# Performance work log

Hardware: AMD Instinct MI355X
Metric: run time of the kernel (lower is better)

Reference implementation:

```python
import jax, jax.numpy as jnp
import numpy as np

DECAY = 0.8
EPS = 1e-05


def setup_inputs() -> dict:
    key = jax.random.key(0)
    k_x, k_e = jax.random.split(key)
    x = jax.random.normal(k_x, (8, 4096, 256), dtype=jnp.float32)
    embed = jax.random.normal(k_e, (8192, 256), dtype=jnp.float32)
    cluster_size = jnp.zeros((8192,), dtype=jnp.float32)
    embed_avg = embed  # buffer initialized as embed.clone()
    return {"x": x, "embed": embed, "cluster_size": cluster_size, "embed_avg": embed_avg}


def reference(x, embed, cluster_size, embed_avg):
    shape = x.shape
    K, d = embed.shape
    flatten = x.reshape(-1, d)  # [N, d]

    dist = -(jnp.sum(flatten * flatten, axis=1, keepdims=True)
             - 2.0 * (flatten @ embed.T)
             + jnp.sum(embed * embed, axis=1)[None, :])  # [N, K]
    embed_ind = jnp.argmax(dist, axis=-1)  # [N]

    quantize = jnp.take(embed, embed_ind, axis=0).reshape(shape)
    embed_ind_out = embed_ind.reshape(shape[:-1])

    # Training-mode EMA update (one_hot sum / one_hot matmul expressed as scatter-adds)
    counts = jnp.zeros((K,), dtype=x.dtype).at[embed_ind].add(1.0)  # embed_onehot.sum(0)
    embed_sum = jnp.zeros((K, d), dtype=x.dtype).at[embed_ind].add(flatten)  # (flatten^T @ onehot)^T

    new_cluster_size = cluster_size * DECAY + counts * (1.0 - DECAY)
    new_embed_avg = embed_avg * DECAY + embed_sum * (1.0 - DECAY)

    smoothed = (new_cluster_size + EPS) / (new_cluster_size.sum() + K * EPS) * new_cluster_size.sum()
    new_embed = new_embed_avg / smoothed[:, None]

    return quantize, embed_ind_out, new_cluster_size, new_embed_avg, new_embed
```

## Files before the change

kernel.cpp:

```cpp
#include <hip/hip_runtime.h>

#define N_ROWS 32768
#define DIM    256
#define KCODES 8192
#define DECAYF 0.8f
#define OMDF   0.2f
#define EPSF   1e-5f

#define Q_OFF    0
#define IND_OFF  8388608
#define CS_OFF   8421376
#define EA_OFF   8429568
#define NE_OFF   10526720


#define WS_E2    0
#define WS_CNT   8192
#define WS_START 16384
#define WS_CUR   24576
#define WS_SUM   40960

typedef _Float16 half8 __attribute__((ext_vector_type(8)));
typedef float floatx16 __attribute__((ext_vector_type(16)));

#define GLOAD16(g, l) __builtin_amdgcn_global_load_lds( \
    (const __attribute__((address_space(1))) void*)(g), \
    (__attribute__((address_space(3))) void*)(l), 16, 0, 0)

#define PREP_ROWS 32
__global__ void prep_all_kernel(const float* __restrict__ x,
                                const float* __restrict__ embed,
                                const float* __restrict__ cs,
                                _Float16* __restrict__ Xp,
                                _Float16* __restrict__ Ep,
                                float* __restrict__ out,
                                float* __restrict__ ws) {
  __shared__ __align__(16) _Float16 L[PREP_ROWS][264];
  __shared__ float red[4];
  const int t = threadIdx.x;
  const int bid = blockIdx.x;

  if (bid < 1024) {
    if (bid < 128) {
      unsigned long long* gbest = (unsigned long long*)(out + EA_OFF);
      gbest[bid * 256 + t] = 0ULL;
    } else if (bid < 160) {
      ((int*)(ws + WS_CNT))[(bid - 128) * 256 + t] = 0;
    }
    const int row0 = bid * PREP_ROWS;
    #pragma unroll
    for (int it = 0; it < 8; ++it) {
      int idx = it * 256 + t;
      int r = idx >> 6, q = idx & 63;
      float4 v = *(const float4*)&x[(size_t)(row0 + r) * DIM + q * 4];
      L[r][q * 4 + 0] = (_Float16)v.x;
      L[r][q * 4 + 1] = (_Float16)v.y;
      L[r][q * 4 + 2] = (_Float16)v.z;
      L[r][q * 4 + 3] = (_Float16)v.w;
    }
    __syncthreads();
    #pragma unroll
    for (int it = 0; it < 4; ++it) {
      int idx = it * 256 + t;
      int slot = idx >> 5, r = idx & 31;
      *(float4*)&Xp[((size_t)slot * N_ROWS + row0 + r) * 8] =
          *(const float4*)&L[r][slot * 8];
    }
  } else {
    const int row0 = (bid - 1024) * PREP_ROWS;
    float* e2 = ws + WS_E2;
    #pragma unroll
    for (int it = 0; it < 8; ++it) {
      int idx = it * 256 + t;
      int r = idx >> 6, q = idx & 63;
      float4 v = *(const float4*)&embed[(size_t)(row0 + r) * DIM + q * 4];
      L[r][q * 4 + 0] = (_Float16)v.x;
      L[r][q * 4 + 1] = (_Float16)v.y;
      L[r][q * 4 + 2] = (_Float16)v.z;
      L[r][q * 4 + 3] = (_Float16)v.w;
      float ssq = v.x * v.x + v.y * v.y + v.z * v.z + v.w * v.w;
      #pragma unroll
      for (int o = 32; o; o >>= 1) ssq += __shfl_xor(ssq, o);
      if ((t & 63) == 0) e2[row0 + r] = ssq;
    }
    if (bid == 1024) {
      float s = 0.0f;
      for (int j = t; j < KCODES; j += 256) s += cs[j];
      #pragma unroll
      for (int o = 32; o; o >>= 1) s += __shfl_xor(s, o);
      if ((t & 63) == 0) red[t >> 6] = s;
    }
    __syncthreads();
    if (bid == 1024 && t == 0)
      ws[WS_SUM] = red[0] + red[1] + red[2] + red[3];
    #pragma unroll
    for (int it = 0; it < 4; ++it) {
      int idx = it * 256 + t;
      int slot = idx >> 5, r = idx & 31;
      *(float4*)&Ep[((size_t)slot * KCODES + row0 + r) * 8] =
          *(const float4*)&L[r][slot * 8];
    }
  }
}

__global__ __launch_bounds__(512, 2) void main_kernel(
    const _Float16* __restrict__ Xp, const _Float16* __restrict__ Ep,
    const float* __restrict__ e2, unsigned long long* __restrict__ gbest) {
  __shared__ __align__(16) _Float16 As[4 * 2 * 256 * 8];
  __shared__ __align__(16) _Float16 Bs[4 * 2 * 256 * 8];
  __shared__ __align__(16) float e2s[256];

  const int t = threadIdx.x;
  const int w = t >> 6;
  const int lane = t & 63;
  const int l31 = lane & 31;
  const int h = lane >> 5;
  const int wm = w >> 2;
  const int wn = w & 3;

  const int bid = blockIdx.x;
  const int bi = bid >> 3;
  const int cb = (bid & 7) * 4 + (bi >> 5);
  const int rbg = bi & 31;
  const int codes0 = cb * 256;
  const int rowbase = rbg * 1024;

  const bool isA = (w < 4);
  const int ws4 = isA ? w : (w - 4);
  const int sl = ws4 >> 1;
  const int qh = ws4 & 1;

  auto stage = [&](int s) {
    const int buf = s & 3;
    const int se = (s & 15) * 2 + sl;
    if (isA) {
      const _Float16* src =
          Ep + ((size_t)se * KCODES + codes0 + qh * 128 + lane) * 8;
      _Float16* dst = &As[buf * 4096 + sl * 2048 + qh * 1024];
      GLOAD16(src, dst);
      GLOAD16(src + 512, dst + 512);
    } else {
      const int row0 = rowbase + (s >> 4) * 256;
      const _Float16* src =
          Xp + ((size_t)se * N_ROWS + row0 + qh * 128 + lane) * 8;
      _Float16* dst = &Bs[buf * 4096 + sl * 2048 + qh * 1024];
      GLOAD16(src, dst);
      GLOAD16(src + 512, dst + 512);
    }
  };

  if (t < 64) {
    float4 v = *(const float4*)&e2[codes0 + t * 4];
    *(float4*)&e2s[t * 4] = v;
  }
  __builtin_amdgcn_sched_barrier(0);
  stage(0);
  stage(1);
  asm volatile("s_waitcnt vmcnt(2)" ::: "memory");
  asm volatile("s_waitcnt lgkmcnt(0)" ::: "memory");
  __builtin_amdgcn_s_barrier();
  __builtin_amdgcn_sched_barrier(0);

  floatx16 acc[4][2];
  unsigned long long pbest[4][2];

  #pragma unroll
  for (int tile = 0; tile < 4; ++tile) {
    #pragma unroll
    for (int ct = 0; ct < 4; ++ct) {
      const int cl = wm * 128 + ct * 32 + 4 * h;
      #pragma unroll
      for (int rq = 0; rq < 4; ++rq) {
        float4 v = *(const float4*)&e2s[cl + rq * 8];
        acc[ct][0][rq * 4 + 0] = -0.5f * v.x;
        acc[ct][0][rq * 4 + 1] = -0.5f * v.y;
        acc[ct][0][rq * 4 + 2] = -0.5f * v.z;
        acc[ct][0][rq * 4 + 3] = -0.5f * v.w;
      }
      acc[ct][1] = acc[ct][0];
    }

    #pragma unroll 1
    for (int i = 0; i < 16; ++i) {
      const int s = tile * 16 + i;
      if (s + 2 < 64) stage(s + 2);
      __builtin_amdgcn_sched_barrier(0);

      const int sbase = (s & 3) * 4096 + h * 2048;
      half8 a0 = *(const half8*)&As[sbase + (wm * 128 + l31) * 8];
      half8 a1 = *(const half8*)&As[sbase + (wm * 128 + 32 + l31) * 8];
      half8 a2 = *(const half8*)&As[sbase + (wm * 128 + 64 + l31) * 8];
      half8 a3 = *(const half8*)&As[sbase + (wm * 128 + 96 + l31) * 8];
      half8 b0 = *(const half8*)&Bs[sbase + (wn * 64 + l31) * 8];
      half8 b1 = *(const half8*)&Bs[sbase + (wn * 64 + 32 + l31) * 8];
      __builtin_amdgcn_s_setprio(1);
      acc[0][0] = __builtin_amdgcn_mfma_f32_32x32x16_f16(a0, b0, acc[0][0], 0, 0, 0);
      acc[0][1] = __builtin_amdgcn_mfma_f32_32x32x16_f16(a0, b1, acc[0][1], 0, 0, 0);
      acc[1][0] = __builtin_amdgcn_mfma_f32_32x32x16_f16(a1, b0, acc[1][0], 0, 0, 0);
      acc[1][1] = __builtin_amdgcn_mfma_f32_32x32x16_f16(a1, b1, acc[1][1], 0, 0, 0);
      acc[2][0] = __builtin_amdgcn_mfma_f32_32x32x16_f16(a2, b0, acc[2][0], 0, 0, 0);
      acc[2][1] = __builtin_amdgcn_mfma_f32_32x32x16_f16(a2, b1, acc[2][1], 0, 0, 0);
      acc[3][0] = __builtin_amdgcn_mfma_f32_32x32x16_f16(a3, b0, acc[3][0], 0, 0, 0);
      acc[3][1] = __builtin_amdgcn_mfma_f32_32x32x16_f16(a3, b1, acc[3][1], 0, 0, 0);
      __builtin_amdgcn_s_setprio(0);
      __builtin_amdgcn_sched_barrier(0);

      if (s < 63) {
        if (s < 62) {
          asm volatile("s_waitcnt vmcnt(2)" ::: "memory");
        } else {
          asm volatile("s_waitcnt vmcnt(0)" ::: "memory");
        }
        __builtin_amdgcn_s_barrier();
        __builtin_amdgcn_sched_barrier(0);
      }
    }

    #pragma unroll
    for (int rt = 0; rt < 2; ++rt) {
      float best = -3.0e38f;
      int bidx = 0;
      #pragma unroll
      for (int ct = 0; ct < 4; ++ct) {
        const int cbase = codes0 + wm * 128 + ct * 32 + 4 * h;
        #pragma unroll
        for (int r = 0; r < 16; ++r) {
          const int code = cbase + (r & 3) + 8 * (r >> 2);
          float v = acc[ct][rt][r];
          if (v > best || (v == best && code < bidx)) { best = v; bidx = code; }
        }
      }
      unsigned u = __float_as_uint(best);
      u = (u & 0x80000000u) ? ~u : (u | 0x80000000u);
      unsigned long long p =
          ((unsigned long long)u << 32) | (unsigned)(8191 - bidx);
      unsigned long long op = (unsigned long long)__shfl_xor((long long)p, 32);
      if (op > p) p = op;
      pbest[tile][rt] = p;
    }
  }

  #pragma unroll
  for (int tile = 0; tile < 4; ++tile)
    #pragma unroll
    for (int rt = 0; rt < 2; ++rt)
      if (h == 0)
        atomicMax(&gbest[rowbase + tile * 256 + wn * 64 + rt * 32 + l31],
                  pbest[tile][rt]);
}

__global__ void decode_count_kernel(const unsigned long long* __restrict__ gbest,
                                    float* __restrict__ out,
                                    int* __restrict__ cnt) {
  int r = blockIdx.x * blockDim.x + threadIdx.x;
  unsigned long long p = gbest[r];
  int k = 8191 - (int)(unsigned)(p & 0xFFFFFFFFull);
  out[IND_OFF + r] = (float)k;
  atomicAdd(&cnt[k], 1);
}

__global__ void prefix_kernel(const int* __restrict__ cnt,
                              int* __restrict__ start,
                              int* __restrict__ cursor) {
  __shared__ int part[1024];
  const int t = threadIdx.x;
  int loc[8];
  int s = 0;
  #pragma unroll
  for (int j = 0; j < 8; ++j) { loc[j] = cnt[t * 8 + j]; s += loc[j]; }
  part[t] = s;
  __syncthreads();
  for (int off = 1; off < 1024; off <<= 1) {
    int v = (t >= off) ? part[t - off] : 0;
    __syncthreads();
    part[t] += v;
    __syncthreads();
  }
  int base = part[t] - s;
  #pragma unroll
  for (int j = 0; j < 8; ++j) {
    start[t * 8 + j] = base;
    cursor[t * 8 + j] = base;
    base += loc[j];
  }
}

__global__ void scatter_rows_kernel(const float* __restrict__ out,
                                    int* __restrict__ cursor,
                                    int* __restrict__ rowlist) {
  int r = blockIdx.x * blockDim.x + threadIdx.x;
  int k = (int)out[IND_OFF + r];
  int pos = atomicAdd(&cursor[k], 1);
  rowlist[pos] = r;
}

__global__ void bucket_final_kernel(const float* __restrict__ x,
                                    const float* __restrict__ cs,
                                    const float* __restrict__ embed_avg,
                                    const int* __restrict__ start,
                                    const int* __restrict__ cnt,
                                    const int* __restrict__ rowlist,
                                    float* __restrict__ out,
                                    const float* __restrict__ ws_sum) {
  const int lane = threadIdx.x & 63;
  const int k = blockIdx.x * 4 + (threadIdx.x >> 6);
  const int s = start[k];
  const int n = cnt[k];
  float4 acc = make_float4(0.f, 0.f, 0.f, 0.f);
  int i = 0;
  for (; i + 2 <= n; i += 2) {
    int r0 = rowlist[s + i];
    int r1 = rowlist[s + i + 1];
    float4 v0 = *(const float4*)&x[(size_t)r0 * DIM + lane * 4];
    float4 v1 = *(const float4*)&x[(size_t)r1 * DIM + lane * 4];
    acc.x += v0.x + v1.x; acc.y += v0.y + v1.y;
    acc.z += v0.z + v1.z; acc.w += v0.w + v1.w;
  }
  if (i < n) {
    int r0 = rowlist[s + i];
    float4 v0 = *(const float4*)&x[(size_t)r0 * DIM + lane * 4];
    acc.x += v0.x; acc.y += v0.y; acc.z += v0.z; acc.w += v0.w;
  }
  const float S = DECAYF * (*ws_sum) + OMDF * (float)N_ROWS;
  const float scale = S / (S + (float)KCODES * EPSF);
  float ncs = cs[k] * DECAYF + (float)n * OMDF;
  if (lane == 0) out[CS_OFF + k] = ncs;
  float4 ea = *(const float4*)&embed_avg[(size_t)k * DIM + lane * 4];
  float4 nea;
  nea.x = ea.x * DECAYF + acc.x * OMDF;
  nea.y = ea.y * DECAYF + acc.y * OMDF;
  nea.z = ea.z * DECAYF + acc.z * OMDF;
  nea.w = ea.w * DECAYF + acc.w * OMDF;
  *(float4*)&out[EA_OFF + (size_t)k * DIM + lane * 4] = nea;
  float inv_sm = 1.0f / ((ncs + EPSF) * scale);
  float4 ne;
  ne.x = nea.x * inv_sm;
  ne.y = nea.y * inv_sm;
  ne.z = nea.z * inv_sm;
  ne.w = nea.w * inv_sm;
  *(float4*)&out[NE_OFF + (size_t)k * DIM + lane * 4] = ne;
}

__global__ void finish_q_kernel(const float* __restrict__ embed,
                                float* __restrict__ out) {
  const int lane = threadIdx.x & 63;
  const int wave = (blockIdx.x * blockDim.x + threadIdx.x) >> 6;
  for (int row = wave; row < N_ROWS; row += 2048) {
    int k = (int)out[IND_OFF + row];
    float4 ev = *(const float4*)&embed[(size_t)k * DIM + lane * 4];
    *(float4*)&out[Q_OFF + (size_t)row * DIM + lane * 4] = ev;
  }
}

extern "C" void kernel_launch(void* const* d_in, const int* in_sizes, int n_in,
                              void* d_out, int out_size, void* d_ws, size_t ws_size,
                              hipStream_t stream) {
  const float* x = (const float*)d_in[0];
  const float* embed = (const float*)d_in[1];
  const float* cs = (const float*)d_in[2];
  const float* ea = (const float*)d_in[3];
  float* out = (float*)d_out;
  float* ws = (float*)d_ws;

  float* e2 = ws + WS_E2;
  int* cnt = (int*)(ws + WS_CNT);
  int* start = (int*)(ws + WS_START);
  int* cursor = (int*)(ws + WS_CUR);
  float* ws_sum = ws + WS_SUM;

  _Float16* Xp = (_Float16*)(out + Q_OFF);
  int* rowlist = (int*)(out + Q_OFF + 4194304);
  unsigned long long* gbest = (unsigned long long*)(out + EA_OFF);
  _Float16* Ep = (_Float16*)(out + EA_OFF + 65536);

  prep_all_kernel<<<1280, 256, 0, stream>>>(x, embed, cs, Xp, Ep, out, ws);
  main_kernel<<<1024, 512, 0, stream>>>(Xp, Ep, e2, gbest);
  decode_count_kernel<<<128, 256, 0, stream>>>(gbest, out, cnt);
  prefix_kernel<<<1, 1024, 0, stream>>>(cnt, start, cursor);
  scatter_rows_kernel<<<128, 256, 0, stream>>>(out, cursor, rowlist);
  bucket_final_kernel<<<2048, 256, 0, stream>>>(x, cs, ea, start, cnt,
                                                rowlist, out, ws_sum);
  finish_q_kernel<<<512, 256, 0, stream>>>(embed, out);
}
```

Baseline: 393.9 us.

## Shrink main kernel row tile to 128 and raise occupancy to four blocks per CU

The GEMM+argmax kernel now tiles 256 codes by 128 rows instead of 256x256, uses a 4x2 warp layout with 2x2 MFMA accumulators per warp, and shrinks the B LDS buffer. Each block covers 2048 rows across 16 tiles, the grid halves to 512 blocks, and launch bounds go from 2 to 4 blocks per CU. Atomic max writes now happen after each tile. This lowers register and LDS use to allow more waves per CU and better latency hiding. The cost is lower MFMA-to-load reuse per step, since each A fragment feeds fewer MFMAs, plus an extra vmcnt(0) drain at every tile boundary.

```diff
diff --git a/kernel.cpp b/kernel.cpp
--- a/kernel.cpp
+++ b/kernel.cpp
@@ -103,11 +103,11 @@
   }
 }
 
-__global__ __launch_bounds__(512, 2) void main_kernel(
+__global__ __launch_bounds__(512, 4) void main_kernel(
     const _Float16* __restrict__ Xp, const _Float16* __restrict__ Ep,
     const float* __restrict__ e2, unsigned long long* __restrict__ gbest) {
   __shared__ __align__(16) _Float16 As[4 * 2 * 256 * 8];
-  __shared__ __align__(16) _Float16 Bs[4 * 2 * 256 * 8];
+  __shared__ __align__(16) _Float16 Bs[4 * 2 * 128 * 8];
   __shared__ __align__(16) float e2s[256];
 
   const int t = threadIdx.x;
@@ -115,37 +115,38 @@
   const int lane = t & 63;
   const int l31 = lane & 31;
   const int h = lane >> 5;
-  const int wm = w >> 2;
-  const int wn = w & 3;
+  const int wm = w >> 1;
+  const int wn = w & 1;
 
   const int bid = blockIdx.x;
   const int bi = bid >> 3;
-  const int cb = (bid & 7) * 4 + (bi >> 5);
-  const int rbg = bi & 31;
+  const int cb = (bid & 7) * 4 + (bi >> 4);
+  const int rg = bi & 15;
   const int codes0 = cb * 256;
-  const int rowbase = rbg * 1024;
+  const int rowbase = rg * 2048;
 
   const bool isA = (w < 4);
-  const int ws4 = isA ? w : (w - 4);
-  const int sl = ws4 >> 1;
-  const int qh = ws4 & 1;
-
-  auto stage = [&](int s) {
-    const int buf = s & 3;
-    const int se = (s & 15) * 2 + sl;
+  const int v4 = isA ? w : (w - 4);
+  const int sl = v4 >> 1;
+  const int hf = v4 & 1;
+
+  const _Float16* estage =
+      Ep + ((size_t)sl * KCODES + codes0 + hf * 128 + lane) * 8;
+  const _Float16* xstage =
+      Xp + ((size_t)sl * N_ROWS + rowbase + hf * 64 + lane) * 8;
+  _Float16* adst = &As[sl * 2048 + (hf * 128 + lane) * 8];
+  _Float16* bdst = &Bs[sl * 1024 + (hf * 64 + lane) * 8];
+
+  auto stage = [&](int buf, int stepk, int rowT) {
     if (isA) {
-      const _Float16* src =
-          Ep + ((size_t)se * KCODES + codes0 + qh * 128 + lane) * 8;
-      _Float16* dst = &As[buf * 4096 + sl * 2048 + qh * 1024];
+      const _Float16* src = estage + (size_t)stepk * 2 * (KCODES * 8);
+      _Float16* dst = adst + buf * 4096;
       GLOAD16(src, dst);
       GLOAD16(src + 512, dst + 512);
     } else {
-      const int row0 = rowbase + (s >> 4) * 256;
       const _Float16* src =
-          Xp + ((size_t)se * N_ROWS + row0 + qh * 128 + lane) * 8;
-      _Float16* dst = &Bs[buf * 4096 + sl * 2048 + qh * 1024];
-      GLOAD16(src, dst);
-      GLOAD16(src + 512, dst + 512);
+          xstage + (size_t)stepk * 2 * (N_ROWS * 8) + (size_t)rowT * 1024;
+      GLOAD16(src, bdst + buf * 2048);
     }
   };
 
@@ -154,21 +155,24 @@
     *(float4*)&e2s[t * 4] = v;
   }
   __builtin_amdgcn_sched_barrier(0);
-  stage(0);
-  stage(1);
-  asm volatile("s_waitcnt vmcnt(2)" ::: "memory");
+  stage(0, 0, 0);
+  stage(1, 1, 0);
+  if (isA) {
+    asm volatile("s_waitcnt vmcnt(2)" ::: "memory");
+  } else {
+    asm volatile("s_waitcnt vmcnt(1)" ::: "memory");
+  }
   asm volatile("s_waitcnt lgkmcnt(0)" ::: "memory");
   __builtin_amdgcn_s_barrier();
   __builtin_amdgcn_sched_barrier(0);
 
-  floatx16 acc[4][2];
-  unsigned long long pbest[4][2];
-
-  #pragma unroll
-  for (int tile = 0; tile < 4; ++tile) {
-    #pragma unroll
-    for (int ct = 0; ct < 4; ++ct) {
-      const int cl = wm * 128 + ct * 32 + 4 * h;
+  floatx16 acc[2][2];
+
+  #pragma unroll 1
+  for (int tile = 0; tile < 16; ++tile) {
+    #pragma unroll
+    for (int ct = 0; ct < 2; ++ct) {
+      const int cl = wm * 64 + ct * 32 + 4 * h;
       #pragma unroll
       for (int rq = 0; rq < 4; ++rq) {
         float4 v = *(const float4*)&e2s[cl + rq * 8];
@@ -180,34 +184,39 @@
       acc[ct][1] = acc[ct][0];
     }
 
-    #pragma unroll 1
+    const bool lastTile = (tile == 15);
+    #pragma unroll
     for (int i = 0; i < 16; ++i) {
-      const int s = tile * 16 + i;
-      if (s + 2 < 64) stage(s + 2);
+      if (!(lastTile && i >= 14)) {
+        const int ip = i + 2;
+        stage(ip & 3, ip & 15, tile + (ip >> 4));
+      }
       __builtin_amdgcn_sched_barrier(0);
 
-      const int sbase = (s & 3) * 4096 + h * 2048;
-      half8 a0 = *(const half8*)&As[sbase + (wm * 128 + l31) * 8];
-      half8 a1 = *(const half8*)&As[sbase + (wm * 128 + 32 + l31) * 8];
-      half8 a2 = *(const half8*)&As[sbase + (wm * 128 + 64 + l31) * 8];
-      half8 a3 = *(const half8*)&As[sbase + (wm * 128 + 96 + l31) * 8];
-      half8 b0 = *(const half8*)&Bs[sbase + (wn * 64 + l31) * 8];
-      half8 b1 = *(const half8*)&Bs[sbase + (wn * 64 + 32 + l31) * 8];
+      const int buf = i & 3;
+      half8 a0 = *(const half8*)&As[buf * 4096 + h * 2048 +
+                                    (wm * 64 + l31) * 8];
+      half8 a1 = *(const half8*)&As[buf * 4096 + h * 2048 +
+                                    (wm * 64 + 32 + l31) * 8];
+      half8 b0 = *(const half8*)&Bs[buf * 2048 + h * 1024 +
+                                    (wn * 64 + l31) * 8];
+      half8 b1 = *(const half8*)&Bs[buf * 2048 + h * 1024 +
+                                    (wn * 64 + 32 + l31) * 8];
       __builtin_amdgcn_s_setprio(1);
       acc[0][0] = __builtin_amdgcn_mfma_f32_32x32x16_f16(a0, b0, acc[0][0], 0, 0, 0);
       acc[0][1] = __builtin_amdgcn_mfma_f32_32x32x16_f16(a0, b1, acc[0][1], 0, 0, 0);
       acc[1][0] = __builtin_amdgcn_mfma_f32_32x32x16_f16(a1, b0, acc[1][0], 0, 0, 0);
       acc[1][1] = __builtin_amdgcn_mfma_f32_32x32x16_f16(a1, b1, acc[1][1], 0, 0, 0);
-      acc[2][0] = __builtin_amdgcn_mfma_f32_32x32x16_f16(a2, b0, acc[2][0], 0, 0, 0);
-      acc[2][1] = __builtin_amdgcn_mfma_f32_32x32x16_f16(a2, b1, acc[2][1], 0, 0, 0);
-      acc[3][0] = __builtin_amdgcn_mfma_f32_32x32x16_f16(a3, b0, acc[3][0], 0, 0, 0);
-      acc[3][1] = __builtin_amdgcn_mfma_f32_32x32x16_f16(a3, b1, acc[3][1], 0, 0, 0);
       __builtin_amdgcn_s_setprio(0);
       __builtin_amdgcn_sched_barrier(0);
 
-      if (s < 63) {
-        if (s < 62) {
-          asm volatile("s_waitcnt vmcnt(2)" ::: "memory");
+      if (!(lastTile && i == 15)) {
+        if (!(lastTile && i == 14)) {
+          if (isA) {
+            asm volatile("s_waitcnt vmcnt(2)" ::: "memory");
+          } else {
+            asm volatile("s_waitcnt vmcnt(1)" ::: "memory");
+          }
         } else {
           asm volatile("s_waitcnt vmcnt(0)" ::: "memory");
         }
@@ -221,8 +230,8 @@
       float best = -3.0e38f;
       int bidx = 0;
       #pragma unroll
-      for (int ct = 0; ct < 4; ++ct) {
-        const int cbase = codes0 + wm * 128 + ct * 32 + 4 * h;
+      for (int ct = 0; ct < 2; ++ct) {
+        const int cbase = codes0 + wm * 64 + ct * 32 + 4 * h;
         #pragma unroll
         for (int r = 0; r < 16; ++r) {
           const int code = cbase + (r & 3) + 8 * (r >> 2);
@@ -236,17 +245,14 @@
           ((unsigned long long)u << 32) | (unsigned)(8191 - bidx);
       unsigned long long op = (unsigned long long)__shfl_xor((long long)p, 32);
       if (op > p) p = op;
-      pbest[tile][rt] = p;
-    }
-  }
-
-  #pragma unroll
-  for (int tile = 0; tile < 4; ++tile)
-    #pragma unroll
-    for (int rt = 0; rt < 2; ++rt)
       if (h == 0)
-        atomicMax(&gbest[rowbase + tile * 256 + wn * 64 + rt * 32 + l31],
-                  pbest[tile][rt]);
+        atomicMax(&gbest[rowbase + tile * 128 + wn * 64 + rt * 32 + l31], p);
+    }
+    if (!lastTile) {
+      asm volatile("s_waitcnt vmcnt(0)" ::: "memory");
+      __builtin_amdgcn_sched_barrier(0);
+    }
+  }
 }
 
 __global__ void decode_count_kernel(const unsigned long long* __restrict__ gbest,
@@ -374,7 +380,7 @@
   _Float16* Ep = (_Float16*)(out + EA_OFF + 65536);
 
   prep_all_kernel<<<1280, 256, 0, stream>>>(x, embed, cs, Xp, Ep, out, ws);
-  main_kernel<<<1024, 512, 0, stream>>>(Xp, Ep, e2, gbest);
+  main_kernel<<<512, 512, 0, stream>>>(Xp, Ep, e2, gbest);
   decode_count_kernel<<<128, 256, 0, stream>>>(gbest, out, cnt);
   prefix_kernel<<<1, 1024, 0, stream>>>(cnt, start, cursor);
   scatter_rows_kernel<<<128, 256, 0, stream>>>(out, cursor, rowlist);
```

New measurement: 395.1 us. No clear change (+0.3%).

## Load GEMM fragments directly from global into registers, drop LDS staging

Applied to the files above, without the earlier changes.

Replaces the LDS-staged, barrier-synchronised four-buffer pipeline in the distance GEMM with per-wave direct global loads of half8 fragments into registers, double-buffered two steps ahead. Each block now computes a single 256x256 tile and the grid is enlarged fourfold, removing the loop over four row tiles. This aims to remove LDS traffic and workgroup barriers, but duplicates global/L2 reads across waves and relies on the cache to absorb the reuse.

```diff
diff --git a/kernel.cpp b/kernel.cpp
--- a/kernel.cpp
+++ b/kernel.cpp
@@ -22,10 +22,6 @@
 
 typedef _Float16 half8 __attribute__((ext_vector_type(8)));
 typedef float floatx16 __attribute__((ext_vector_type(16)));
-
-#define GLOAD16(g, l) __builtin_amdgcn_global_load_lds( \
-    (const __attribute__((address_space(1))) void*)(g), \
-    (__attribute__((address_space(3))) void*)(l), 16, 0, 0)
 
 #define PREP_ROWS 32
 __global__ void prep_all_kernel(const float* __restrict__ x,
@@ -106,10 +102,6 @@
 __global__ __launch_bounds__(512, 2) void main_kernel(
     const _Float16* __restrict__ Xp, const _Float16* __restrict__ Ep,
     const float* __restrict__ e2, unsigned long long* __restrict__ gbest) {
-  __shared__ __align__(16) _Float16 As[4 * 2 * 256 * 8];
-  __shared__ __align__(16) _Float16 Bs[4 * 2 * 256 * 8];
-  __shared__ __align__(16) float e2s[256];
-
   const int t = threadIdx.x;
   const int w = t >> 6;
   const int lane = t & 63;
@@ -120,133 +112,88 @@
 
   const int bid = blockIdx.x;
   const int bi = bid >> 3;
-  const int cb = (bid & 7) * 4 + (bi >> 5);
-  const int rbg = bi & 31;
+  const int cb = (bid & 7) * 4 + (bi >> 7);
+  const int rb = bi & 127;
   const int codes0 = cb * 256;
-  const int rowbase = rbg * 1024;
-
-  const bool isA = (w < 4);
-  const int ws4 = isA ? w : (w - 4);
-  const int sl = ws4 >> 1;
-  const int qh = ws4 & 1;
-
-  auto stage = [&](int s) {
-    const int buf = s & 3;
-    const int se = (s & 15) * 2 + sl;
-    if (isA) {
-      const _Float16* src =
-          Ep + ((size_t)se * KCODES + codes0 + qh * 128 + lane) * 8;
-      _Float16* dst = &As[buf * 4096 + sl * 2048 + qh * 1024];
-      GLOAD16(src, dst);
-      GLOAD16(src + 512, dst + 512);
-    } else {
-      const int row0 = rowbase + (s >> 4) * 256;
-      const _Float16* src =
-          Xp + ((size_t)se * N_ROWS + row0 + qh * 128 + lane) * 8;
-      _Float16* dst = &Bs[buf * 4096 + sl * 2048 + qh * 1024];
-      GLOAD16(src, dst);
-      GLOAD16(src + 512, dst + 512);
-    }
-  };
-
-  if (t < 64) {
-    float4 v = *(const float4*)&e2[codes0 + t * 4];
-    *(float4*)&e2s[t * 4] = v;
-  }
-  __builtin_amdgcn_sched_barrier(0);
-  stage(0);
-  stage(1);
-  asm volatile("s_waitcnt vmcnt(2)" ::: "memory");
-  asm volatile("s_waitcnt lgkmcnt(0)" ::: "memory");
-  __builtin_amdgcn_s_barrier();
-  __builtin_amdgcn_sched_barrier(0);
+  const int row0 = rb * 256;
+
+  const _Float16* aB = Ep + ((size_t)h * KCODES + codes0 + wm * 128 + l31) * 8;
+  const _Float16* bB = Xp + ((size_t)h * N_ROWS + row0 + wn * 64 + l31) * 8;
+  const size_t aStep = (size_t)2 * KCODES * 8;
+  const size_t bStep = (size_t)2 * N_ROWS * 8;
 
   floatx16 acc[4][2];
-  unsigned long long pbest[4][2];
-
-  #pragma unroll
-  for (int tile = 0; tile < 4; ++tile) {
+  #pragma unroll
+  for (int ct = 0; ct < 4; ++ct) {
+    const int cbase = codes0 + wm * 128 + ct * 32 + 4 * h;
+    #pragma unroll
+    for (int rq = 0; rq < 4; ++rq) {
+      float4 v = *(const float4*)&e2[cbase + rq * 8];
+      acc[ct][0][rq * 4 + 0] = -0.5f * v.x;
+      acc[ct][0][rq * 4 + 1] = -0.5f * v.y;
+      acc[ct][0][rq * 4 + 2] = -0.5f * v.z;
+      acc[ct][0][rq * 4 + 3] = -0.5f * v.w;
+    }
+    acc[ct][1] = acc[ct][0];
+  }
+
+  half8 A[2][4], B[2][2];
+  #pragma unroll
+  for (int p = 0; p < 2; ++p) {
+    #pragma unroll
+    for (int f = 0; f < 4; ++f)
+      A[p][f] = *(const half8*)(aB + (size_t)p * aStep + f * 32 * 8);
+    B[p][0] = *(const half8*)(bB + (size_t)p * bStep);
+    B[p][1] = *(const half8*)(bB + (size_t)p * bStep + 32 * 8);
+  }
+
+  #pragma unroll
+  for (int j = 0; j < 16; ++j) {
+    const int p = j & 1;
+    __builtin_amdgcn_s_setprio(1);
+    acc[0][0] = __builtin_amdgcn_mfma_f32_32x32x16_f16(A[p][0], B[p][0], acc[0][0], 0, 0, 0);
+    acc[0][1] = __builtin_amdgcn_mfma_f32_32x32x16_f16(A[p][0], B[p][1], acc[0][1], 0, 0, 0);
+    acc[1][0] = __builtin_amdgcn_mfma_f32_32x32x16_f16(A[p][1], B[p][0], acc[1][0], 0, 0, 0);
+    acc[1][1] = __builtin_amdgcn_mfma_f32_32x32x16_f16(A[p][1], B[p][1], acc[1][1], 0, 0, 0);
+    acc[2][0] = __builtin_amdgcn_mfma_f32_32x32x16_f16(A[p][2], B[p][0], acc[2][0], 0, 0, 0);
+    acc[2][1] = __builtin_amdgcn_mfma_f32_32x32x16_f16(A[p][2], B[p][1], acc[2][1], 0, 0, 0);
+    acc[3][0] = __builtin_amdgcn_mfma_f32_32x32x16_f16(A[p][3], B[p][0], acc[3][0], 0, 0, 0);
+    acc[3][1] = __builtin_amdgcn_mfma_f32_32x32x16_f16(A[p][3], B[p][1], acc[3][1], 0, 0, 0);
+    __builtin_amdgcn_s_setprio(0);
+    if (j + 2 < 16) {
+      const size_t ja = (size_t)(j + 2) * aStep;
+      const size_t jb = (size_t)(j + 2) * bStep;
+      #pragma unroll
+      for (int f = 0; f < 4; ++f)
+        A[p][f] = *(const half8*)(aB + ja + f * 32 * 8);
+      B[p][0] = *(const half8*)(bB + jb);
+      B[p][1] = *(const half8*)(bB + jb + 32 * 8);
+    }
+  }
+
+  #pragma unroll
+  for (int rt = 0; rt < 2; ++rt) {
+    float best = -3.0e38f;
+    int bidx = 0;
     #pragma unroll
     for (int ct = 0; ct < 4; ++ct) {
-      const int cl = wm * 128 + ct * 32 + 4 * h;
+      const int cbase = codes0 + wm * 128 + ct * 32 + 4 * h;
       #pragma unroll
-      for (int rq = 0; rq < 4; ++rq) {
-        float4 v = *(const float4*)&e2s[cl + rq * 8];
-        acc[ct][0][rq * 4 + 0] = -0.5f * v.x;
-        acc[ct][0][rq * 4 + 1] = -0.5f * v.y;
-        acc[ct][0][rq * 4 + 2] = -0.5f * v.z;
-        acc[ct][0][rq * 4 + 3] = -0.5f * v.w;
+      for (int r = 0; r < 16; ++r) {
+        const int code = cbase + (r & 3) + 8 * (r >> 2);
+        float v = acc[ct][rt][r];
+        if (v > best || (v == best && code < bidx)) { best = v; bidx = code; }
       }
-      acc[ct][1] = acc[ct][0];
-    }
-
-    #pragma unroll 1
-    for (int i = 0; i < 16; ++i) {
-      const int s = tile * 16 + i;
-      if (s + 2 < 64) stage(s + 2);
-      __builtin_amdgcn_sched_barrier(0);
-
-      const int sbase = (s & 3) * 4096 + h * 2048;
-      half8 a0 = *(const half8*)&As[sbase + (wm * 128 + l31) * 8];
-      half8 a1 = *(const half8*)&As[sbase + (wm * 128 + 32 + l31) * 8];
-      half8 a2 = *(const half8*)&As[sbase + (wm * 128 + 64 + l31) * 8];
-      half8 a3 = *(const half8*)&As[sbase + (wm * 128 + 96 + l31) * 8];
-      half8 b0 = *(const half8*)&Bs[sbase + (wn * 64 + l31) * 8];
-      half8 b1 = *(const half8*)&Bs[sbase + (wn * 64 + 32 + l31) * 8];
-      __builtin_amdgcn_s_setprio(1);
-      acc[0][0] = __builtin_amdgcn_mfma_f32_32x32x16_f16(a0, b0, acc[0][0], 0, 0, 0);
-      acc[0][1] = __builtin_amdgcn_mfma_f32_32x32x16_f16(a0, b1, acc[0][1], 0, 0, 0);
-      acc[1][0] = __builtin_amdgcn_mfma_f32_32x32x16_f16(a1, b0, acc[1][0], 0, 0, 0);
-      acc[1][1] = __builtin_amdgcn_mfma_f32_32x32x16_f16(a1, b1, acc[1][1], 0, 0, 0);
-      acc[2][0] = __builtin_amdgcn_mfma_f32_32x32x16_f16(a2, b0, acc[2][0], 0, 0, 0);
-      acc[2][1] = __builtin_amdgcn_mfma_f32_32x32x16_f16(a2, b1, acc[2][1], 0, 0, 0);
-      acc[3][0] = __builtin_amdgcn_mfma_f32_32x32x16_f16(a3, b0, acc[3][0], 0, 0, 0);
-      acc[3][1] = __builtin_amdgcn_mfma_f32_32x32x16_f16(a3, b1, acc[3][1], 0, 0, 0);
-      __builtin_amdgcn_s_setprio(0);
-      __builtin_amdgcn_sched_barrier(0);
-
-      if (s < 63) {
-        if (s < 62) {
-          asm volatile("s_waitcnt vmcnt(2)" ::: "memory");
-        } else {
-          asm volatile("s_waitcnt vmcnt(0)" ::: "memory");
-        }
-        __builtin_amdgcn_s_barrier();
-        __builtin_amdgcn_sched_barrier(0);
-      }
-    }
-
-    #pragma unroll
-    for (int rt = 0; rt < 2; ++rt) {
-      float best = -3.0e38f;
-      int bidx = 0;
-      #pragma unroll
-      for (int ct = 0; ct < 4; ++ct) {
-        const int cbase = codes0 + wm * 128 + ct * 32 + 4 * h;
-        #pragma unroll
-        for (int r = 0; r < 16; ++r) {
-          const int code = cbase + (r & 3) + 8 * (r >> 2);
-          float v = acc[ct][rt][r];
-          if (v > best || (v == best && code < bidx)) { best = v; bidx = code; }
-        }
-      }
-      unsigned u = __float_as_uint(best);
-      u = (u & 0x80000000u) ? ~u : (u | 0x80000000u);
-      unsigned long long p =
-          ((unsigned long long)u << 32) | (unsigned)(8191 - bidx);
-      unsigned long long op = (unsigned long long)__shfl_xor((long long)p, 32);
-      if (op > p) p = op;
-      pbest[tile][rt] = p;
-    }
-  }
-
-  #pragma unroll
-  for (int tile = 0; tile < 4; ++tile)
-    #pragma unroll
-    for (int rt = 0; rt < 2; ++rt)
-      if (h == 0)
-        atomicMax(&gbest[rowbase + tile * 256 + wn * 64 + rt * 32 + l31],
-                  pbest[tile][rt]);
+    }
+    unsigned u = __float_as_uint(best);
+    u = (u & 0x80000000u) ? ~u : (u | 0x80000000u);
+    unsigned long long p =
+        ((unsigned long long)u << 32) | (unsigned)(8191 - bidx);
+    unsigned long long op = (unsigned long long)__shfl_xor((long long)p, 32);
+    if (op > p) p = op;
+    if (h == 0)
+      atomicMax(&gbest[row0 + wn * 64 + rt * 32 + l31], p);
+  }
 }
 
 __global__ void decode_count_kernel(const unsigned long long* __restrict__ gbest,
@@ -374,7 +321,7 @@
   _Float16* Ep = (_Float16*)(out + EA_OFF + 65536);
 
   prep_all_kernel<<<1280, 256, 0, stream>>>(x, embed, cs, Xp, Ep, out, ws);
-  main_kernel<<<1024, 512, 0, stream>>>(Xp, Ep, e2, gbest);
+  main_kernel<<<4096, 512, 0, stream>>>(Xp, Ep, e2, gbest);
   decode_count_kernel<<<128, 256, 0, stream>>>(gbest, out, cnt);
   prefix_kernel<<<1, 1024, 0, stream>>>(cnt, start, cursor);
   scatter_rows_kernel<<<128, 256, 0, stream>>>(out, cursor, rowlist);
```

Measured after the change: 407.1 us. 1.03x slower.
